# Kernel tuning notes

Measured on AMD Instinct MI355X. Metric: run time of the kernel, lower is better.

## Reference

```python
import jax, jax.numpy as jnp
import numpy as np
import math

D_MODEL = 1024
D_STATE = 16
D_CONV = 4
EXPAND = 2
D_INNER = EXPAND * D_MODEL
DT_RANK = math.ceil(D_MODEL / 16)
EPS = 1e-5


def setup_inputs() -> dict:
    key = jax.random.key(0)
    ks = jax.random.split(key, 8)
    B, L = 2, 1024
    s = 0.02
    return {
        "hidden_states": jax.random.normal(ks[0], (B, L, D_MODEL), jnp.float32),
        "norm_weight": jnp.ones((D_MODEL,), jnp.float32),
        "in_proj_w": (jax.random.normal(ks[1], (2 * D_INNER, D_MODEL), jnp.float32) * s),
        "conv_w": (jax.random.normal(ks[2], (D_INNER, D_CONV), jnp.float32) * s),
        "conv_b": jnp.zeros((D_INNER,), jnp.float32),
        "x_proj_w": (jax.random.normal(ks[3], (DT_RANK + 2 * D_STATE, D_INNER), jnp.float32) * s),
        "dt_proj_w": (jax.random.normal(ks[4], (D_INNER, DT_RANK), jnp.float32) * s),
        "dt_proj_b": jax.random.uniform(ks[5], (D_INNER,), jnp.float32, -4.0, -2.0),
        "A_log": jnp.log(jnp.broadcast_to(jnp.arange(1, D_STATE + 1, dtype=jnp.float32), (D_INNER, D_STATE))),
        "D": jnp.ones((D_INNER,), jnp.float32),
        "out_proj_w": (jax.random.normal(ks[6], (D_MODEL, D_INNER), jnp.float32) * s),
    }


def _rmsnorm(x, w):
    # Faithful to source: rms = ||x||_2 / sqrt(d); x / (rms + eps) * w
    norm = jnp.linalg.norm(x, axis=-1, keepdims=True)
    rms = norm * (1.0 / math.sqrt(x.shape[-1]))
    return w * (x / (rms + EPS))


def _mamba(h, in_proj_w, conv_w, conv_b, x_proj_w, dt_proj_w, dt_proj_b, A_log, D, out_proj_w):
    B, L, _ = h.shape
    xz = h @ in_proj_w.T                      # (B,L,2*D_INNER)
    x, z = jnp.split(xz, 2, axis=-1)          # each (B,L,D_INNER)

    # causal depthwise conv1d along L, kernel D_CONV
    xpad = jnp.pad(x, ((0, 0), (D_CONV - 1, 0), (0, 0)))
    xc = conv_b
    for k in range(D_CONV):                   # tiny fixed loop over kernel taps
        xc = xc + xpad[:, k:k + L, :] * conv_w[:, k]
    xc = jax.nn.silu(xc)                      # (B,L,D_INNER)

    x_dbl = xc @ x_proj_w.T                   # (B,L,DT_RANK+2N)
    dt, Bm, Cm = jnp.split(x_dbl, [DT_RANK, DT_RANK + D_STATE], axis=-1)
    dt = jax.nn.softplus(dt @ dt_proj_w.T + dt_proj_b)   # (B,L,D_INNER)

    A = -jnp.exp(A_log)                       # (D_INNER,N)
    deltaA = jnp.exp(dt[..., None] * A)                      # (B,L,D_INNER,N)
    deltaBu = (dt * xc)[..., None] * Bm[:, :, None, :]        # (B,L,D_INNER,N)

    def step(hst, inp):
        dA, dBu, Ct = inp
        hst = dA * hst + dBu                  # (B,D_INNER,N)
        y = jnp.einsum('bdn,bn->bd', hst, Ct)
        return hst, y

    h0 = jnp.zeros((B, D_INNER, D_STATE), xc.dtype)
    _, ys = jax.lax.scan(step, h0, (deltaA.swapaxes(0, 1), deltaBu.swapaxes(0, 1), Cm.swapaxes(0, 1)))
    y = ys.swapaxes(0, 1)                     # (B,L,D_INNER)
    y = y + D * xc
    y = y * jax.nn.silu(z)
    return y @ out_proj_w.T                   # (B,L,D_MODEL)


def reference(hidden_states, norm_weight, in_proj_w, conv_w, conv_b, x_proj_w,
              dt_proj_w, dt_proj_b, A_log, D, out_proj_w):
    residual = hidden_states
    h = _rmsnorm(residual, norm_weight)
    out = _mamba(h, in_proj_w, conv_w, conv_b, x_proj_w, dt_proj_w, dt_proj_b,
                 A_log, D, out_proj_w)
    return out, residual
```

## Files before the change

kernel.cpp:

```cpp
#include <hip/hip_runtime.h>

typedef __bf16 bf16x8 __attribute__((ext_vector_type(8)));
typedef float f32x4 __attribute__((ext_vector_type(4)));

__device__ __forceinline__ float b2f(ushort u) {
    union { unsigned int i; float f; } v;
    v.i = ((unsigned int)u) << 16;
    return v.f;
}
__device__ __forceinline__ ushort f2b(float f) {
    union { float f; unsigned int i; } v;
    v.f = f;
    unsigned int x = v.i;
    unsigned int r = (x + 0x7fffu + ((x >> 16) & 1u)) >> 16;
    return (ushort)r;
}
__device__ __forceinline__ void gload16(const ushort* g, ushort* l) {
    __builtin_amdgcn_global_load_lds(
        (const __attribute__((address_space(1))) unsigned int*)g,
        (__attribute__((address_space(3))) unsigned int*)l, 16, 0, 0);
}
__device__ __forceinline__ bf16x8 ldsfrag(const ushort* s, int row, int cq) {
    int p = cq ^ (row & 7);
    return *(const bf16x8*)(s + row * 64 + p * 8);
}

#define D_MODEL 1024
#define D_INNER 2048
#define D_STATE 16
#define DT_RANK 64
#define NTOK    2048
#define LSEQ    1024
#define NCH     32
#define LC      32
#define KSL     16

__global__ __launch_bounds__(256) void prep_kernel(
    const float* __restrict__ hs, const float* __restrict__ w,
    ushort* __restrict__ hout, float* __restrict__ resid,
    const float* __restrict__ inproj, const float* __restrict__ outproj,
    const float* __restrict__ xprojw, const float* __restrict__ dtw,
    ushort* __restrict__ wIn, ushort* __restrict__ wOut,
    ushort* __restrict__ xpw, ushort* __restrict__ dtwb)
{
    int blk = blockIdx.x;
    int tid = threadIdx.x;
    if (blk < NTOK) {
        int t = blk;
        float4 r4 = *(const float4*)(hs + (size_t)t * D_MODEL + tid * 4);
        float s = r4.x * r4.x + r4.y * r4.y + r4.z * r4.z + r4.w * r4.w;
        #pragma unroll
        for (int off = 32; off >= 1; off >>= 1) s += __shfl_xor(s, off);
        __shared__ float red[4];
        int lane = tid & 63, wid = tid >> 6;
        if (lane == 0) red[wid] = s;
        __syncthreads();
        float tot = red[0] + red[1] + red[2] + red[3];
        float inv = 1.0f / (sqrtf(tot) * (1.0f / 32.0f) + 1e-5f);
        float4 w4 = *(const float4*)(w + tid * 4);
        ushort4 o;
        o.x = f2b(w4.x * r4.x * inv);
        o.y = f2b(w4.y * r4.y * inv);
        o.z = f2b(w4.z * r4.z * inv);
        o.w = f2b(w4.w * r4.w * inv);
        *(ushort4*)(hout + (size_t)t * D_MODEL + tid * 4) = o;
        *(float4*)(resid + (size_t)t * D_MODEL + tid * 4) = r4;
    } else {
        int i = (blk - NTOK) * 256 + tid;
        const float* src; ushort* dst; int off;
        if (i < 1048576)      { src = inproj;  dst = wIn;  off = i; }
        else if (i < 1572864) { src = outproj; dst = wOut; off = i - 1048576; }
        else if (i < 1622016) { src = xprojw;  dst = xpw;  off = i - 1572864; }
        else if (i < 1654784) { src = dtw;     dst = dtwb; off = i - 1622016; }
        else return;
        float4 v = *(const float4*)(src + (size_t)off * 4);
        ushort4 o;
        o.x = f2b(v.x); o.y = f2b(v.y); o.z = f2b(v.z); o.w = f2b(v.w);
        *(ushort4*)(dst + (size_t)off * 4) = o;
    }
}

__global__ __launch_bounds__(256) void gemm_xz_kernel(
    const ushort* __restrict__ Ag, const ushort* __restrict__ Wg,
    ushort* __restrict__ xq, ushort* __restrict__ zq, int K)
{
    __shared__ __align__(16) ushort sA[128 * 64];
    __shared__ __align__(16) ushort sB[128 * 64];
    int tid = threadIdx.x;
    int bm = blockIdx.x, bn = blockIdx.y;
    int wid = tid >> 6, lane = tid & 63;
    int wm = (wid >> 1) * 64, wn = (wid & 1) * 64;
    int l16 = lane & 15, q = lane >> 4;

    f32x4 acc[4][4];
    #pragma unroll
    for (int i = 0; i < 4; i++)
        #pragma unroll
        for (int j = 0; j < 4; j++)
            acc[i][j] = (f32x4){0.f, 0.f, 0.f, 0.f};

    const ushort* Abase = Ag + (size_t)bm * 128 * K;
    const ushort* Wbase = Wg + (size_t)bn * 128 * K;

    int segr = lane >> 3, segc = lane & 7;
    size_t goff[4]; int sseg[4];
    #pragma unroll
    for (int t = 0; t < 4; t++) {
        int s = wid * 4 + t;
        int r = s * 8 + segr;
        int gc = segc ^ (r & 7);
        sseg[t] = s * 512;
        goff[t] = (size_t)r * K + gc * 8;
    }

    for (int k0 = 0; k0 < K; k0 += 64) {
        __syncthreads();
        #pragma unroll
        for (int t = 0; t < 4; t++) {
            gload16(Abase + goff[t] + k0, sA + sseg[t]);
            gload16(Wbase + goff[t] + k0, sB + sseg[t]);
        }
        __syncthreads();
        #pragma unroll
        for (int ks = 0; ks < 2; ks++) {
            int cq = ks * 4 + q;
            bf16x8 af[4], bfr[4];
            #pragma unroll
            for (int i = 0; i < 4; i++)
                af[i] = ldsfrag(sA, wm + i * 16 + l16, cq);
            #pragma unroll
            for (int j = 0; j < 4; j++)
                bfr[j] = ldsfrag(sB, wn + j * 16 + l16, cq);
            #pragma unroll
            for (int i = 0; i < 4; i++)
                #pragma unroll
                for (int j = 0; j < 4; j++)
                    acc[i][j] = __builtin_amdgcn_mfma_f32_16x16x32_bf16(af[i], bfr[j], acc[i][j], 0, 0, 0);
        }
    }

    ushort* dst = (bn < 16) ? xq : zq;
    int row0 = bm * 128 + wm + q * 4;
    int col0 = (bn & 15) * 128 + wn + l16;
    #pragma unroll
    for (int i = 0; i < 4; i++)
        #pragma unroll
        for (int j = 0; j < 4; j++)
            #pragma unroll
            for (int r = 0; r < 4; r++)
                dst[(size_t)(row0 + i * 16 + r) * D_INNER + col0 + j * 16] =
                    f2b(acc[i][j][r]);
}

__global__ __launch_bounds__(256) void gemm64_kernel(
    const ushort* __restrict__ Ag, const ushort* __restrict__ Wg,
    float* __restrict__ Cf, int M, int N, int K)
{
    __shared__ __align__(16) ushort sA[64 * 64];
    __shared__ __align__(16) ushort sB[64 * 64];
    int tid = threadIdx.x;
    int bm = blockIdx.x, bn = blockIdx.y;
    int wid = tid >> 6, lane = tid & 63;
    int wm = wid * 16;
    int l16 = lane & 15, q = lane >> 4;

    f32x4 acc[4];
    #pragma unroll
    for (int j = 0; j < 4; j++) acc[j] = (f32x4){0.f, 0.f, 0.f, 0.f};

    const ushort* Abase = Ag + (size_t)bm * 64 * K;
    const ushort* Wbase = Wg + (size_t)bn * 64 * K;

    int segr = lane >> 3, segc = lane & 7;
    size_t goff[2]; int sseg[2];
    #pragma unroll
    for (int t = 0; t < 2; t++) {
        int s = wid * 2 + t;
        int r = s * 8 + segr;
        int gc = segc ^ (r & 7);
        sseg[t] = s * 512;
        goff[t] = (size_t)r * K + gc * 8;
    }

    for (int k0 = 0; k0 < K; k0 += 64) {
        __syncthreads();
        #pragma unroll
        for (int t = 0; t < 2; t++) {
            gload16(Abase + goff[t] + k0, sA + sseg[t]);
            gload16(Wbase + goff[t] + k0, sB + sseg[t]);
        }
        __syncthreads();
        #pragma unroll
        for (int ks = 0; ks < 2; ks++) {
            int cq = ks * 4 + q;
            bf16x8 af = ldsfrag(sA, wm + l16, cq);
            bf16x8 bfr[4];
            #pragma unroll
            for (int j = 0; j < 4; j++)
                bfr[j] = ldsfrag(sB, j * 16 + l16, cq);
            #pragma unroll
            for (int j = 0; j < 4; j++)
                acc[j] = __builtin_amdgcn_mfma_f32_16x16x32_bf16(af, bfr[j], acc[j], 0, 0, 0);
        }
    }

    int row0 = bm * 64 + wm + q * 4;
    int col0 = bn * 64 + l16;
    #pragma unroll
    for (int j = 0; j < 4; j++)
        #pragma unroll
        for (int r = 0; r < 4; r++)
            Cf[(size_t)(row0 + r) * N + col0 + j * 16] = acc[j][r];
}

__global__ __launch_bounds__(256) void conv_silu_kernel(
    const ushort* __restrict__ xq, const float* __restrict__ cw,
    const float* __restrict__ cb, ushort* __restrict__ xcb)
{
    int idx = blockIdx.x * 256 + threadIdx.x;
    int d = idx & (D_INNER - 1);
    int t = idx >> 11;
    int l = t & (LSEQ - 1), b = t >> 10;
    float4 w4 = *(const float4*)(cw + d * 4);
    float acc = cb[d];
    float wk[4] = {w4.x, w4.y, w4.z, w4.w};
    #pragma unroll
    for (int k = 0; k < 4; k++) {
        int ll = l - 3 + k;
        float xv = (ll >= 0) ? b2f(xq[(((size_t)(b * LSEQ + ll)) << 11) + d]) : 0.f;
        acc += xv * wk[k];
    }
    float sg = acc / (1.f + __expf(-acc));
    xcb[idx] = f2b(sg);
}

__global__ __launch_bounds__(256) void xproj_partial_kernel(
    const ushort* __restrict__ xcb, const ushort* __restrict__ wq,
    float* __restrict__ partials)
{
    __shared__ __align__(16) ushort sA[128 * 32];
    __shared__ __align__(16) ushort sB[96 * 32];
    int tid = threadIdx.x;
    int bm = blockIdx.x, sl = blockIdx.y;
    int wid = tid >> 6, lane = tid & 63;
    int wm = wid * 32;
    int l16 = lane & 15, q = lane >> 4;

    f32x4 acc[2][6];
    #pragma unroll
    for (int i = 0; i < 2; i++)
        #pragma unroll
        for (int j = 0; j < 6; j++)
            acc[i][j] = (f32x4){0.f, 0.f, 0.f, 0.f};

    const ushort* Abase = xcb + (size_t)bm * 128 * D_INNER;
    int kbase = sl * (D_INNER / KSL);

    for (int kk = 0; kk < D_INNER / KSL; kk += 32) {
        int k0 = kbase + kk;
        __syncthreads();
        #pragma unroll
        for (int i = tid; i < 512; i += 256) {
            int r = i >> 2, c = (i & 3) << 3;
            *(uint4*)(sA + i * 8) = *(const uint4*)(Abase + (size_t)r * D_INNER + k0 + c);
        }
        for (int i = tid; i < 384; i += 256) {
            int r = i >> 2, c = (i & 3) << 3;
            *(uint4*)(sB + i * 8) = *(const uint4*)(wq + (size_t)r * D_INNER + k0 + c);
        }
        __syncthreads();
        bf16x8 af[2], bfr[6];
        #pragma unroll
        for (int i = 0; i < 2; i++)
            af[i] = *(const bf16x8*)(sA + (wm + i * 16 + l16) * 32 + q * 8);
        #pragma unroll
        for (int j = 0; j < 6; j++)
            bfr[j] = *(const bf16x8*)(sB + (j * 16 + l16) * 32 + q * 8);
        #pragma unroll
        for (int i = 0; i < 2; i++)
            #pragma unroll
            for (int j = 0; j < 6; j++)
                acc[i][j] = __builtin_amdgcn_mfma_f32_16x16x32_bf16(af[i], bfr[j], acc[i][j], 0, 0, 0);
    }

    float* out = partials + (size_t)sl * NTOK * 96;
    int row0 = bm * 128 + wm + q * 4;
    #pragma unroll
    for (int i = 0; i < 2; i++)
        #pragma unroll
        for (int j = 0; j < 6; j++)
            #pragma unroll
            for (int r = 0; r < 4; r++)
                out[(size_t)(row0 + i * 16 + r) * 96 + j * 16 + l16] = acc[i][j][r];
}

__global__ __launch_bounds__(256) void xproj_reduce_kernel(
    const float* __restrict__ partials, float* __restrict__ xdbl,
    ushort* __restrict__ xdbl64)
{
    int idx = blockIdx.x * 256 + threadIdx.x;
    float s = 0.f;
    #pragma unroll
    for (int sl = 0; sl < KSL; sl++)
        s += partials[(size_t)sl * NTOK * 96 + idx];
    xdbl[idx] = s;
    int col = idx % 96;
    if (col < DT_RANK)
        xdbl64[(size_t)(idx / 96) * DT_RANK + col] = f2b(s);
}

__global__ __launch_bounds__(256) void dt_gemm_kernel(
    const ushort* __restrict__ xd64, const ushort* __restrict__ dtwq,
    const float* __restrict__ dtb, ushort* __restrict__ dtout)
{
    __shared__ __align__(16) ushort sA[64 * 72];
    __shared__ __align__(16) ushort sB[64 * 72];
    int tid = threadIdx.x;
    int bm = blockIdx.x, bn = blockIdx.y;
    int wid = tid >> 6, lane = tid & 63;
    int wm = wid * 16;
    int l16 = lane & 15, q = lane >> 4;

    const ushort* Abase = xd64 + (size_t)bm * 64 * DT_RANK;
    const ushort* Bbase = dtwq + (size_t)bn * 64 * DT_RANK;
    #pragma unroll
    for (int i = tid; i < 512; i += 256) {
        int r = i >> 3, c = (i & 7) << 3;
        *(uint4*)(sA + r * 72 + c) = *(const uint4*)(Abase + (size_t)r * DT_RANK + c);
        *(uint4*)(sB + r * 72 + c) = *(const uint4*)(Bbase + (size_t)r * DT_RANK + c);
    }
    __syncthreads();

    f32x4 acc[4];
    #pragma unroll
    for (int j = 0; j < 4; j++) acc[j] = (f32x4){0.f, 0.f, 0.f, 0.f};

    #pragma unroll
    for (int ks = 0; ks < 2; ks++) {
        bf16x8 af = *(const bf16x8*)(sA + (wm + l16) * 72 + ks * 32 + q * 8);
        bf16x8 bfr[4];
        #pragma unroll
        for (int j = 0; j < 4; j++)
            bfr[j] = *(const bf16x8*)(sB + (j * 16 + l16) * 72 + ks * 32 + q * 8);
        #pragma unroll
        for (int j = 0; j < 4; j++)
            acc[j] = __builtin_amdgcn_mfma_f32_16x16x32_bf16(af, bfr[j], acc[j], 0, 0, 0);
    }

    __syncthreads();
    #pragma unroll
    for (int j = 0; j < 4; j++) {
        float bias = dtb[bn * 64 + j * 16 + l16];
        #pragma unroll
        for (int r = 0; r < 4; r++) {
            float s = acc[j][r] + bias;
            float sp = (s > 20.f) ? s : log1pf(__expf(s));
            sA[(wm + q * 4 + r) * 72 + j * 16 + l16] = f2b(sp);
        }
    }
    __syncthreads();
    int row0 = bm * 64, col0 = bn * 64;
    #pragma unroll
    for (int rep = 0; rep < 2; rep++) {
        int off = rep * 2048 + tid * 8;
        int row = off >> 6, col = off & 63;
        *(uint4*)(dtout + (size_t)(row0 + row) * D_INNER + col0 + col) =
            *(const uint4*)(sA + row * 72 + col);
    }
}

__global__ __launch_bounds__(256) void scan_partA_kernel(
    const ushort* __restrict__ dt, const ushort* __restrict__ xcq,
    const float* __restrict__ xdbl, const float* __restrict__ Alog,
    float2* __restrict__ ch1, float2* __restrict__ ch2)
{
    __shared__ float sBC[LC][32];
    int bid = blockIdx.x;
    int g = bid & 7;
    int c = (bid >> 3) & (NCH - 1);
    int b = bid >> 8;
    int tid = threadIdx.x;
    int lane = tid & 63, wid = tid >> 6;
    int d = g * 256 + wid * 64 + lane;
    int l0 = c * LC;

    {
        int r = tid >> 3, c4 = (tid & 7) * 4;
        *(float4*)&sBC[r][c4] =
            *(const float4*)(xdbl + ((size_t)(b * LSEQ + l0 + r)) * 96 + 64 + c4);
    }
    float A[16];
    #pragma unroll
    for (int k = 0; k < 4; k++)
        *(float4*)&A[k * 4] = *(const float4*)(Alog + d * D_STATE + k * 4);
    #pragma unroll
    for (int n = 0; n < 16; n++) A[n] = -__expf(A[n]);
    __syncthreads();

    const ushort* dtp = dt  + ((size_t)(b * LSEQ + l0)) * D_INNER + d;
    const ushort* xcp = xcq + ((size_t)(b * LSEQ + l0)) * D_INNER + d;

    float h[16], ap[16];
    #pragma unroll
    for (int n = 0; n < 16; n++) { h[n] = 0.f; ap[n] = 1.f; }

    for (int l = 0; l < LC; l++) {
        float dtv = b2f(dtp[(size_t)l * D_INNER]);
        float xcv = b2f(xcp[(size_t)l * D_INNER]);
        float t = dtv * xcv;
        float Bv[16];
        #pragma unroll
        for (int k = 0; k < 4; k++)
            *(float4*)&Bv[k * 4] = *(const float4*)&sBC[l][k * 4];
        #pragma unroll
        for (int n = 0; n < 16; n++) {
            float a = __expf(dtv * A[n]);
            h[n] = h[n] * a + t * Bv[n];
            ap[n] *= a;
        }
    }

    float2* outp = (c < 16 ? ch1 : ch2) +
                   ((size_t)((b * 16 + (c & 15)) * D_INNER + d)) * D_STATE;
    #pragma unroll
    for (int n = 0; n < 16; n += 2) {
        float4 v = {ap[n], h[n], ap[n + 1], h[n + 1]};
        *(float4*)&outp[n] = v;
    }
}

__global__ __launch_bounds__(256) void scan_partB_kernel(
    float2* __restrict__ ch1, float2* __restrict__ ch2)
{
    int kk = blockIdx.x * 256 + threadIdx.x;
    int b = kk >> 15, dn = kk & 32767;
    float run = 0.f;
    #pragma unroll
    for (int c = 0; c < NCH; c++) {
        float2* p = (c < 16 ? ch1 : ch2) +
                    (size_t)(b * 16 + (c & 15)) * 32768 + dn;
        float2 v = *p;
        p->x = run;
        run = v.x * run + v.y;
    }
}

__global__ __launch_bounds__(256) void scan_partC_kernel(
    const ushort* __restrict__ dt, const ushort* __restrict__ xcq,
    const float* __restrict__ xdbl, const ushort* __restrict__ zq,
    const float* __restrict__ Alog, const float* __restrict__ Dp,
    const float2* __restrict__ ch1, const float2* __restrict__ ch2,
    ushort* __restrict__ yg)
{
    __shared__ float sBC[LC][32];
    int bid = blockIdx.x;
    int g = bid & 7;
    int c = (bid >> 3) & (NCH - 1);
    int b = bid >> 8;
    int tid = threadIdx.x;
    int lane = tid & 63, wid = tid >> 6;
    int d = g * 256 + wid * 64 + lane;
    int l0 = c * LC;

    {
        int r = tid >> 3, c4 = (tid & 7) * 4;
        *(float4*)&sBC[r][c4] =
            *(const float4*)(xdbl + ((size_t)(b * LSEQ + l0 + r)) * 96 + 64 + c4);
    }
    float A[16];
    #pragma unroll
    for (int k = 0; k < 4; k++)
        *(float4*)&A[k * 4] = *(const float4*)(Alog + d * D_STATE + k * 4);
    #pragma unroll
    for (int n = 0; n < 16; n++) A[n] = -__expf(A[n]);
    float Dd = Dp[d];

    const float2* hip_ = (c < 16 ? ch1 : ch2) +
                         ((size_t)((b * 16 + (c & 15)) * D_INNER + d)) * D_STATE;
    float h[16];
    #pragma unroll
    for (int n = 0; n < 16; n += 2) {
        float4 v = *(const float4*)&hip_[n];
        h[n] = v.x; h[n + 1] = v.z;
    }
    __syncthreads();

    const ushort* dtp = dt  + ((size_t)(b * LSEQ + l0)) * D_INNER + d;
    const ushort* xcp = xcq + ((size_t)(b * LSEQ + l0)) * D_INNER + d;
    const ushort* zp  = zq  + ((size_t)(b * LSEQ + l0)) * D_INNER + d;
    ushort* yp = yg + ((size_t)(b * LSEQ + l0)) * D_INNER + d;

    for (int l = 0; l < LC; l++) {
        float dtv = b2f(dtp[(size_t)l * D_INNER]);
        float xcv = b2f(xcp[(size_t)l * D_INNER]);
        float zv  = b2f(zp[(size_t)l * D_INNER]);
        float t = dtv * xcv;
        float Bv[16], Cv[16];
        #pragma unroll
        for (int k = 0; k < 4; k++) {
            *(float4*)&Bv[k * 4] = *(const float4*)&sBC[l][k * 4];
            *(float4*)&Cv[k * 4] = *(const float4*)&sBC[l][16 + k * 4];
        }
        float p0 = 0.f, p1 = 0.f, p2 = 0.f, p3 = 0.f;
        #pragma unroll
        for (int n = 0; n < 16; n += 4) {
            float a0 = __expf(dtv * A[n]);
            float a1 = __expf(dtv * A[n + 1]);
            float a2 = __expf(dtv * A[n + 2]);
            float a3 = __expf(dtv * A[n + 3]);
            h[n]     = h[n] * a0 + t * Bv[n];
            h[n + 1] = h[n + 1] * a1 + t * Bv[n + 1];
            h[n + 2] = h[n + 2] * a2 + t * Bv[n + 2];
            h[n + 3] = h[n + 3] * a3 + t * Bv[n + 3];
            p0 += h[n] * Cv[n];
            p1 += h[n + 1] * Cv[n + 1];
            p2 += h[n + 2] * Cv[n + 2];
            p3 += h[n + 3] * Cv[n + 3];
        }
        float p = (p0 + p1) + (p2 + p3);
        float y = p + Dd * xcv;
        float sz = zv / (1.f + __expf(-zv));
        yp[(size_t)l * D_INNER] = f2b(y * sz);
    }
}

extern "C" void kernel_launch(void* const* d_in, const int* in_sizes, int n_in,
                              void* d_out, int out_size, void* d_ws, size_t ws_size,
                              hipStream_t stream)
{
    const float* hs      = (const float*)d_in[0];
    const float* norm_w  = (const float*)d_in[1];
    const float* inproj  = (const float*)d_in[2];
    const float* convw   = (const float*)d_in[3];
    const float* convb   = (const float*)d_in[4];
    const float* xprojw  = (const float*)d_in[5];
    const float* dtw     = (const float*)d_in[6];
    const float* dtb     = (const float*)d_in[7];
    const float* alog    = (const float*)d_in[8];
    const float* dvec    = (const float*)d_in[9];
    const float* outproj = (const float*)d_in[10];

    float* out_main  = (float*)d_out;
    float* out_resid = (float*)d_out + (size_t)NTOK * D_MODEL;

    char* ws = (char*)d_ws;
    ushort* xq      = (ushort*)(ws);
    ushort* zq      = (ushort*)(ws +  9437184);
    ushort* dtq     = (ushort*)(ws + 18874368);
    float2* ch1     = (float2*)(ws + 28311552);
    float2* ch2     = (float2*)(ws + 37748736);
    float*  xdbl    = (float*) (ws + 47185920);
    ushort* xd64    = (ushort*)(ws + 48234496);
    ushort* xpw_b   = (ushort*)(ws + 48758784);
    ushort* dtw_b   = (ushort*)(ws + 49283072);
    ushort* wIn     = (ushort*)(ws + 50331648);
    ushort* wOut    = (ushort*)(ws + 59768832);
    ushort* h_bf16  = (ushort*)(ws + 65011712);
    float*  xprojP  = (float*) (ws + 70254592);
    ushort* yg_bf16 = (ushort*)(ws + 83886080);
    ushort* xcb     = (ushort*)(ws + 92274688);

    prep_kernel<<<NTOK + 6464, 256, 0, stream>>>(
        hs, norm_w, h_bf16, out_resid,
        inproj, outproj, xprojw, dtw, wIn, wOut, xpw_b, dtw_b);

    gemm_xz_kernel<<<dim3(NTOK / 128, (2 * D_INNER) / 128), 256, 0, stream>>>(
        h_bf16, wIn, xq, zq, D_MODEL);

    conv_silu_kernel<<<(NTOK * D_INNER) / 256, 256, 0, stream>>>(
        xq, convw, convb, xcb);

    xproj_partial_kernel<<<dim3(NTOK / 128, KSL), 256, 0, stream>>>(
        xcb, xpw_b, xprojP);
    xproj_reduce_kernel<<<NTOK * 96 / 256, 256, 0, stream>>>(xprojP, xdbl, xd64);

    dt_gemm_kernel<<<dim3(NTOK / 64, D_INNER / 64), 256, 0, stream>>>(
        xd64, dtw_b, dtb, dtq);

    scan_partA_kernel<<<512, 256, 0, stream>>>(dtq, xcb, xdbl, alog, ch1, ch2);
    scan_partB_kernel<<<256, 256, 0, stream>>>(ch1, ch2);
    scan_partC_kernel<<<512, 256, 0, stream>>>(dtq, xcb, xdbl, zq,
                                               alog, dvec, ch1, ch2, yg_bf16);

    gemm64_kernel<<<dim3(NTOK / 64, D_MODEL / 64), 256, 0, stream>>>(
        yg_bf16, wOut, out_main, NTOK, D_MODEL, D_INNER);
}
```

Baseline: 262.7 us.

## Replace x_proj split-K reduce with atomics, double scan chunks, use exp2

The split-K x_proj partial kernel now accumulates straight into a zeroed xdbl buffer with atomicAdd, so the separate reduce kernel and the partials buffer go away. The zeroing is folded into the prep kernel, and dt_gemm converts fp32 xdbl to bf16 as it loads. The chunked scan now uses 64 chunks of 16 steps instead of 32 of 32, giving twice as many blocks in parts A and C, with a unified chunk-state layout. The A coefficients are pre-scaled by log2(e) so the hardware exp2 can be used. In exchange, atomics make the summation order nondeterministic, and part B's serial pass over chunks is twice as long.

```diff
diff --git a/kernel.cpp b/kernel.cpp
--- a/kernel.cpp
+++ b/kernel.cpp
@@ -15,6 +15,13 @@
     unsigned int r = (x + 0x7fffu + ((x >> 16) & 1u)) >> 16;
     return (ushort)r;
 }
+__device__ __forceinline__ float fexp2(float x) {
+#if __has_builtin(__builtin_amdgcn_exp2f)
+    return __builtin_amdgcn_exp2f(x);
+#else
+    return exp2f(x);
+#endif
+}
 __device__ __forceinline__ void gload16(const ushort* g, ushort* l) {
     __builtin_amdgcn_global_load_lds(
         (const __attribute__((address_space(1))) unsigned int*)g,
@@ -31,9 +38,10 @@
 #define DT_RANK 64
 #define NTOK    2048
 #define LSEQ    1024
-#define NCH     32
-#define LC      32
+#define NCH     64
+#define LC      16
 #define KSL     16
+#define LOG2E   1.44269504088896f
 
 __global__ __launch_bounds__(256) void prep_kernel(
     const float* __restrict__ hs, const float* __restrict__ w,
@@ -41,7 +49,8 @@
     const float* __restrict__ inproj, const float* __restrict__ outproj,
     const float* __restrict__ xprojw, const float* __restrict__ dtw,
     ushort* __restrict__ wIn, ushort* __restrict__ wOut,
-    ushort* __restrict__ xpw, ushort* __restrict__ dtwb)
+    ushort* __restrict__ xpw, ushort* __restrict__ dtwb,
+    float* __restrict__ xdbl)
 {
     int blk = blockIdx.x;
     int tid = threadIdx.x;
@@ -65,7 +74,7 @@
         o.w = f2b(w4.w * r4.w * inv);
         *(ushort4*)(hout + (size_t)t * D_MODEL + tid * 4) = o;
         *(float4*)(resid + (size_t)t * D_MODEL + tid * 4) = r4;
-    } else {
+    } else if (blk < NTOK + 6464) {
         int i = (blk - NTOK) * 256 + tid;
         const float* src; ushort* dst; int off;
         if (i < 1048576)      { src = inproj;  dst = wIn;  off = i; }
@@ -77,6 +86,10 @@
         ushort4 o;
         o.x = f2b(v.x); o.y = f2b(v.y); o.z = f2b(v.z); o.w = f2b(v.w);
         *(ushort4*)(dst + (size_t)off * 4) = o;
+    } else {
+        int i = (blk - NTOK - 6464) * 256 + tid;
+        if (i < 49152)
+            *(float4*)(xdbl + (size_t)i * 4) = (float4){0.f, 0.f, 0.f, 0.f};
     }
 }
 
@@ -236,7 +249,7 @@
 
 __global__ __launch_bounds__(256) void xproj_partial_kernel(
     const ushort* __restrict__ xcb, const ushort* __restrict__ wq,
-    float* __restrict__ partials)
+    float* __restrict__ xdbl)
 {
     __shared__ __align__(16) ushort sA[128 * 32];
     __shared__ __align__(16) ushort sB[96 * 32];
@@ -283,7 +296,6 @@
                 acc[i][j] = __builtin_amdgcn_mfma_f32_16x16x32_bf16(af[i], bfr[j], acc[i][j], 0, 0, 0);
     }
 
-    float* out = partials + (size_t)sl * NTOK * 96;
     int row0 = bm * 128 + wm + q * 4;
     #pragma unroll
     for (int i = 0; i < 2; i++)
@@ -291,26 +303,12 @@
         for (int j = 0; j < 6; j++)
             #pragma unroll
             for (int r = 0; r < 4; r++)
-                out[(size_t)(row0 + i * 16 + r) * 96 + j * 16 + l16] = acc[i][j][r];
-}
-
-__global__ __launch_bounds__(256) void xproj_reduce_kernel(
-    const float* __restrict__ partials, float* __restrict__ xdbl,
-    ushort* __restrict__ xdbl64)
-{
-    int idx = blockIdx.x * 256 + threadIdx.x;
-    float s = 0.f;
-    #pragma unroll
-    for (int sl = 0; sl < KSL; sl++)
-        s += partials[(size_t)sl * NTOK * 96 + idx];
-    xdbl[idx] = s;
-    int col = idx % 96;
-    if (col < DT_RANK)
-        xdbl64[(size_t)(idx / 96) * DT_RANK + col] = f2b(s);
+                atomicAdd(&xdbl[(size_t)(row0 + i * 16 + r) * 96 + j * 16 + l16],
+                          acc[i][j][r]);
 }
 
 __global__ __launch_bounds__(256) void dt_gemm_kernel(
-    const ushort* __restrict__ xd64, const ushort* __restrict__ dtwq,
+    const float* __restrict__ xdbl, const ushort* __restrict__ dtwq,
     const float* __restrict__ dtb, ushort* __restrict__ dtout)
 {
     __shared__ __align__(16) ushort sA[64 * 72];
@@ -321,12 +319,16 @@
     int wm = wid * 16;
     int l16 = lane & 15, q = lane >> 4;
 
-    const ushort* Abase = xd64 + (size_t)bm * 64 * DT_RANK;
+    const float* Abase = xdbl + (size_t)bm * 64 * 96;
     const ushort* Bbase = dtwq + (size_t)bn * 64 * DT_RANK;
     #pragma unroll
     for (int i = tid; i < 512; i += 256) {
         int r = i >> 3, c = (i & 7) << 3;
-        *(uint4*)(sA + r * 72 + c) = *(const uint4*)(Abase + (size_t)r * DT_RANK + c);
+        float4 v0 = *(const float4*)(Abase + (size_t)r * 96 + c);
+        float4 v1 = *(const float4*)(Abase + (size_t)r * 96 + c + 4);
+        ushort o[8] = {f2b(v0.x), f2b(v0.y), f2b(v0.z), f2b(v0.w),
+                       f2b(v1.x), f2b(v1.y), f2b(v1.z), f2b(v1.w)};
+        *(uint4*)(sA + r * 72 + c) = *(const uint4*)o;
         *(uint4*)(sB + r * 72 + c) = *(const uint4*)(Bbase + (size_t)r * DT_RANK + c);
     }
     __syncthreads();
@@ -372,19 +374,19 @@
 __global__ __launch_bounds__(256) void scan_partA_kernel(
     const ushort* __restrict__ dt, const ushort* __restrict__ xcq,
     const float* __restrict__ xdbl, const float* __restrict__ Alog,
-    float2* __restrict__ ch1, float2* __restrict__ ch2)
+    float2* __restrict__ ch)
 {
     __shared__ float sBC[LC][32];
     int bid = blockIdx.x;
     int g = bid & 7;
     int c = (bid >> 3) & (NCH - 1);
-    int b = bid >> 8;
+    int b = bid >> 9;
     int tid = threadIdx.x;
     int lane = tid & 63, wid = tid >> 6;
     int d = g * 256 + wid * 64 + lane;
     int l0 = c * LC;
 
-    {
+    if (tid < LC * 8) {
         int r = tid >> 3, c4 = (tid & 7) * 4;
         *(float4*)&sBC[r][c4] =
             *(const float4*)(xdbl + ((size_t)(b * LSEQ + l0 + r)) * 96 + 64 + c4);
@@ -394,7 +396,7 @@
     for (int k = 0; k < 4; k++)
         *(float4*)&A[k * 4] = *(const float4*)(Alog + d * D_STATE + k * 4);
     #pragma unroll
-    for (int n = 0; n < 16; n++) A[n] = -__expf(A[n]);
+    for (int n = 0; n < 16; n++) A[n] = -__expf(A[n]) * LOG2E;
     __syncthreads();
 
     const ushort* dtp = dt  + ((size_t)(b * LSEQ + l0)) * D_INNER + d;
@@ -414,14 +416,13 @@
             *(float4*)&Bv[k * 4] = *(const float4*)&sBC[l][k * 4];
         #pragma unroll
         for (int n = 0; n < 16; n++) {
-            float a = __expf(dtv * A[n]);
+            float a = fexp2(dtv * A[n]);
             h[n] = h[n] * a + t * Bv[n];
             ap[n] *= a;
         }
     }
 
-    float2* outp = (c < 16 ? ch1 : ch2) +
-                   ((size_t)((b * 16 + (c & 15)) * D_INNER + d)) * D_STATE;
+    float2* outp = ch + (((size_t)(c * 2 + b)) << 15) + (d << 4);
     #pragma unroll
     for (int n = 0; n < 16; n += 2) {
         float4 v = {ap[n], h[n], ap[n + 1], h[n + 1]};
@@ -429,16 +430,14 @@
     }
 }
 
-__global__ __launch_bounds__(256) void scan_partB_kernel(
-    float2* __restrict__ ch1, float2* __restrict__ ch2)
+__global__ __launch_bounds__(256) void scan_partB_kernel(float2* __restrict__ ch)
 {
     int kk = blockIdx.x * 256 + threadIdx.x;
     int b = kk >> 15, dn = kk & 32767;
     float run = 0.f;
-    #pragma unroll
+    #pragma unroll 8
     for (int c = 0; c < NCH; c++) {
-        float2* p = (c < 16 ? ch1 : ch2) +
-                    (size_t)(b * 16 + (c & 15)) * 32768 + dn;
+        float2* p = ch + (((size_t)(c * 2 + b)) << 15) + dn;
         float2 v = *p;
         p->x = run;
         run = v.x * run + v.y;
@@ -449,20 +448,19 @@
     const ushort* __restrict__ dt, const ushort* __restrict__ xcq,
     const float* __restrict__ xdbl, const ushort* __restrict__ zq,
     const float* __restrict__ Alog, const float* __restrict__ Dp,
-    const float2* __restrict__ ch1, const float2* __restrict__ ch2,
-    ushort* __restrict__ yg)
+    const float2* __restrict__ ch, ushort* __restrict__ yg)
 {
     __shared__ float sBC[LC][32];
     int bid = blockIdx.x;
     int g = bid & 7;
     int c = (bid >> 3) & (NCH - 1);
-    int b = bid >> 8;
+    int b = bid >> 9;
     int tid = threadIdx.x;
     int lane = tid & 63, wid = tid >> 6;
     int d = g * 256 + wid * 64 + lane;
     int l0 = c * LC;
 
-    {
+    if (tid < LC * 8) {
         int r = tid >> 3, c4 = (tid & 7) * 4;
         *(float4*)&sBC[r][c4] =
             *(const float4*)(xdbl + ((size_t)(b * LSEQ + l0 + r)) * 96 + 64 + c4);
@@ -472,11 +470,10 @@
     for (int k = 0; k < 4; k++)
         *(float4*)&A[k * 4] = *(const float4*)(Alog + d * D_STATE + k * 4);
     #pragma unroll
-    for (int n = 0; n < 16; n++) A[n] = -__expf(A[n]);
+    for (int n = 0; n < 16; n++) A[n] = -__expf(A[n]) * LOG2E;
     float Dd = Dp[d];
 
-    const float2* hip_ = (c < 16 ? ch1 : ch2) +
-                         ((size_t)((b * 16 + (c & 15)) * D_INNER + d)) * D_STATE;
+    const float2* hip_ = ch + (((size_t)(c * 2 + b)) << 15) + (d << 4);
     float h[16];
     #pragma unroll
     for (int n = 0; n < 16; n += 2) {
@@ -504,10 +501,10 @@
         float p0 = 0.f, p1 = 0.f, p2 = 0.f, p3 = 0.f;
         #pragma unroll
         for (int n = 0; n < 16; n += 4) {
-            float a0 = __expf(dtv * A[n]);
-            float a1 = __expf(dtv * A[n + 1]);
-            float a2 = __expf(dtv * A[n + 2]);
-            float a3 = __expf(dtv * A[n + 3]);
+            float a0 = fexp2(dtv * A[n]);
+            float a1 = fexp2(dtv * A[n + 1]);
+            float a2 = fexp2(dtv * A[n + 2]);
+            float a3 = fexp2(dtv * A[n + 3]);
             h[n]     = h[n] * a0 + t * Bv[n];
             h[n + 1] = h[n + 1] * a1 + t * Bv[n + 1];
             h[n + 2] = h[n + 2] * a2 + t * Bv[n + 2];
@@ -545,24 +542,21 @@
 
     char* ws = (char*)d_ws;
     ushort* xq      = (ushort*)(ws);
-    ushort* zq      = (ushort*)(ws +  9437184);
-    ushort* dtq     = (ushort*)(ws + 18874368);
-    float2* ch1     = (float2*)(ws + 28311552);
-    float2* ch2     = (float2*)(ws + 37748736);
-    float*  xdbl    = (float*) (ws + 47185920);
-    ushort* xd64    = (ushort*)(ws + 48234496);
-    ushort* xpw_b   = (ushort*)(ws + 48758784);
-    ushort* dtw_b   = (ushort*)(ws + 49283072);
-    ushort* wIn     = (ushort*)(ws + 50331648);
-    ushort* wOut    = (ushort*)(ws + 59768832);
-    ushort* h_bf16  = (ushort*)(ws + 65011712);
-    float*  xprojP  = (float*) (ws + 70254592);
-    ushort* yg_bf16 = (ushort*)(ws + 83886080);
-    ushort* xcb     = (ushort*)(ws + 92274688);
-
-    prep_kernel<<<NTOK + 6464, 256, 0, stream>>>(
+    ushort* zq      = (ushort*)(ws +  8388608);
+    ushort* dtq     = (ushort*)(ws + 16777216);
+    ushort* xcb     = (ushort*)(ws + 25165824);
+    float2* ch      = (float2*)(ws + 33554432);
+    float*  xdbl    = (float*) (ws + 67108864);
+    ushort* wIn     = (ushort*)(ws + 67895296);
+    ushort* wOut    = (ushort*)(ws + 76283904);
+    ushort* h_bf16  = (ushort*)(ws + 80478208);
+    ushort* xpw_b   = (ushort*)(ws + 84672512);
+    ushort* dtw_b   = (ushort*)(ws + 85065728);
+    ushort* yg_bf16 = (ushort*)(ws + 85327872);
+
+    prep_kernel<<<NTOK + 6464 + 192, 256, 0, stream>>>(
         hs, norm_w, h_bf16, out_resid,
-        inproj, outproj, xprojw, dtw, wIn, wOut, xpw_b, dtw_b);
+        inproj, outproj, xprojw, dtw, wIn, wOut, xpw_b, dtw_b, xdbl);
 
     gemm_xz_kernel<<<dim3(NTOK / 128, (2 * D_INNER) / 128), 256, 0, stream>>>(
         h_bf16, wIn, xq, zq, D_MODEL);
@@ -571,16 +565,15 @@
         xq, convw, convb, xcb);
 
     xproj_partial_kernel<<<dim3(NTOK / 128, KSL), 256, 0, stream>>>(
-        xcb, xpw_b, xprojP);
-    xproj_reduce_kernel<<<NTOK * 96 / 256, 256, 0, stream>>>(xprojP, xdbl, xd64);
+        xcb, xpw_b, xdbl);
 
     dt_gemm_kernel<<<dim3(NTOK / 64, D_INNER / 64), 256, 0, stream>>>(
-        xd64, dtw_b, dtb, dtq);
-
-    scan_partA_kernel<<<512, 256, 0, stream>>>(dtq, xcb, xdbl, alog, ch1, ch2);
-    scan_partB_kernel<<<256, 256, 0, stream>>>(ch1, ch2);
-    scan_partC_kernel<<<512, 256, 0, stream>>>(dtq, xcb, xdbl, zq,
-                                               alog, dvec, ch1, ch2, yg_bf16);
+        xdbl, dtw_b, dtb, dtq);
+
+    scan_partA_kernel<<<1024, 256, 0, stream>>>(dtq, xcb, xdbl, alog, ch);
+    scan_partB_kernel<<<256, 256, 0, stream>>>(ch);
+    scan_partC_kernel<<<1024, 256, 0, stream>>>(dtq, xcb, xdbl, zq,
+                                                alog, dvec, ch, yg_bf16);
 
     gemm64_kernel<<<dim3(NTOK / 64, D_MODEL / 64), 256, 0, stream>>>(
         yg_bf16, wOut, out_main, NTOK, D_MODEL, D_INNER);
```

Measured after the change: 254.4 us. -3.1%, faster.
